# Optimization experiments

Measured on AMD Instinct MI355X. Metric: run time of the kernel, lower is better.

The kernel has to match this reference:

```python
import jax, jax.numpy as jnp
import numpy as np
import math

B, S, D, H, F = 2, 2048, 1024, 16, 4096
HD = D // H  # head size 64
EPS = 1e-5


def layernorm(x, g, b):
    mu = jnp.mean(x, axis=-1, keepdims=True)
    var = jnp.mean((x - mu) ** 2, axis=-1, keepdims=True)
    return (x - mu) * jax.lax.rsqrt(var + EPS) * g + b


def new_gelu(x):
    c = math.sqrt(2.0 / math.pi)
    return 0.5 * x * (1.0 + jnp.tanh(c * (x + 0.044715 * x ** 3)))


def setup_inputs() -> dict:
    key = jax.random.key(0)
    ks = jax.random.split(key, 20)
    sc = 0.02
    return {
        "x": jax.random.normal(ks[0], (B, S, D), jnp.float32),
        # per-head q/k/v weights stacked: [H, HD, D] (torch Linear weight layout [out,in])
        "Wq": jax.random.normal(ks[1], (H, HD, D), jnp.float32) * sc,
        "bq": jax.random.normal(ks[2], (H, HD), jnp.float32) * sc,
        "Wk": jax.random.normal(ks[3], (H, HD, D), jnp.float32) * sc,
        "bk": jax.random.normal(ks[4], (H, HD), jnp.float32) * sc,
        "Wv": jax.random.normal(ks[5], (H, HD, D), jnp.float32) * sc,
        "bv": jax.random.normal(ks[6], (H, HD), jnp.float32) * sc,
        "Wo": jax.random.normal(ks[7], (D, D), jnp.float32) * sc,
        "bo": jax.random.normal(ks[8], (D,), jnp.float32) * sc,
        "ln1_g": 1.0 + jax.random.normal(ks[9], (D,), jnp.float32) * sc,
        "ln1_b": jax.random.normal(ks[10], (D,), jnp.float32) * sc,
        "W1": jax.random.normal(ks[11], (F, D), jnp.float32) * sc,
        "b1": jax.random.normal(ks[12], (F,), jnp.float32) * sc,
        "W2": jax.random.normal(ks[13], (D, F), jnp.float32) * sc,
        "b2": jax.random.normal(ks[14], (D,), jnp.float32) * sc,
        "ln2_g": 1.0 + jax.random.normal(ks[15], (D,), jnp.float32) * sc,
        "ln2_b": jax.random.normal(ks[16], (D,), jnp.float32) * sc,
    }


def reference(x, Wq, bq, Wk, bk, Wv, bv, Wo, bo, ln1_g, ln1_b, W1, b1, W2, b2, ln2_g, ln2_b):
    # --- pre-LN multi-head attention (dropout is identity in eval) ---
    h = layernorm(x, ln1_g, ln1_b)
    q = jnp.einsum("bsd,hed->bshe", h, Wq) + bq  # [B,S,H,HD]
    k = jnp.einsum("bsd,hed->bshe", h, Wk) + bk
    v = jnp.einsum("bsd,hed->bshe", h, Wv) + bv
    scores = jnp.einsum("bshe,bthe->bhst", q, k) / math.sqrt(HD)
    probs = jax.nn.softmax(scores, axis=-1)
    attn = jnp.einsum("bhst,bthe->bshe", probs, v).reshape(B, S, D)  # concat heads
    attn = attn @ Wo.T + bo
    x = x + attn
    # --- pre-LN MLP with NewGELU ---
    h2 = layernorm(x, ln2_g, ln2_b)
    mlp = new_gelu(h2 @ W1.T + b1) @ W2.T + b2
    return x + mlp
```

## Files before the change

kernel.cpp:

```cpp
#include <hip/hip_runtime.h>

typedef unsigned short u16;
typedef __attribute__((ext_vector_type(8))) __bf16 bf16x8;
typedef __attribute__((ext_vector_type(4))) __bf16 bf16x4;
typedef __attribute__((ext_vector_type(4))) float f32x4;
typedef __attribute__((ext_vector_type(4))) unsigned short u16x4;

#define AS1 __attribute__((address_space(1)))
#define AS3 __attribute__((address_space(3)))

__device__ __forceinline__ void async_load16(const void* g, void* l) {
  __builtin_amdgcn_global_load_lds((const AS1 void*)g, (AS3 void*)l, 16, 0, 0);
}

__device__ __forceinline__ float exp2_fast(float x) {
#if __has_builtin(__builtin_amdgcn_exp2f)
  return __builtin_amdgcn_exp2f(x);
#else
  return exp2f(x);
#endif
}
__device__ __forceinline__ float rcp_fast(float x) {
#if __has_builtin(__builtin_amdgcn_rcpf)
  return __builtin_amdgcn_rcpf(x);
#else
  return 1.0f / x;
#endif
}

__device__ __forceinline__ u16 f2bf(float f) {
  union { float f; unsigned u; } a; a.f = f;
  unsigned u = a.u;
  u += 0x7fffu + ((u >> 16) & 1u);
  return (u16)(u >> 16);
}
__device__ __forceinline__ u16 bf_bits(float f) {
  union { __bf16 b; u16 u; } c; c.b = (__bf16)f; return c.u;
}
__device__ __forceinline__ float bf2f(u16 h) {
  union { unsigned u; float f; } c; c.u = ((unsigned)h) << 16; return c.f;
}

__global__ __launch_bounds__(256)
void f2b_all(const float* __restrict__ s0, const float* __restrict__ s1,
             const float* __restrict__ s2, const float* __restrict__ s3,
             const float* __restrict__ s4, const float* __restrict__ s5,
             u16* __restrict__ dst) {
  const int i = blockIdx.x * 256 + threadIdx.x;
  const float* s; int off;
  if (i < 1048576) {
    if (i < 262144)      { s = s0; off = i; }
    else if (i < 524288) { s = s1; off = i - 262144; }
    else if (i < 786432) { s = s2; off = i - 524288; }
    else                 { s = s3; off = i - 786432; }
  } else if (i < 2097152) { s = s4; off = i - 1048576; }
  else                    { s = s5; off = i - 2097152; }
  const float4 v = ((const float4*)s)[off];
  u16x4 o; o[0] = f2bf(v.x); o[1] = f2bf(v.y); o[2] = f2bf(v.z); o[3] = f2bf(v.w);
  ((u16x4*)dst)[i] = o;
}

__global__ __launch_bounds__(256)
void ln_kernel(const float* __restrict__ x, const float* __restrict__ g,
               const float* __restrict__ b, u16* __restrict__ out) {
  const int row = blockIdx.x, tid = threadIdx.x;
  const float4 v = ((const float4*)(x + (size_t)row * 1024))[tid];
  float s = v.x + v.y + v.z + v.w;
  float s2 = v.x * v.x + v.y * v.y + v.z * v.z + v.w * v.w;
#pragma unroll
  for (int o = 1; o < 64; o <<= 1) { s += __shfl_xor(s, o); s2 += __shfl_xor(s2, o); }
  __shared__ float red[8];
  const int wave = tid >> 6, lane = tid & 63;
  if (lane == 0) { red[wave] = s; red[wave + 4] = s2; }
  __syncthreads();
  s = red[0] + red[1] + red[2] + red[3];
  s2 = red[4] + red[5] + red[6] + red[7];
  const float mu = s * (1.f / 1024.f);
  const float rstd = rsqrtf(s2 * (1.f / 1024.f) - mu * mu + 1e-5f);
  const float4 gg = ((const float4*)g)[tid];
  const float4 bb = ((const float4*)b)[tid];
  u16x4 o4;
  o4[0] = f2bf((v.x - mu) * rstd * gg.x + bb.x);
  o4[1] = f2bf((v.y - mu) * rstd * gg.y + bb.y);
  o4[2] = f2bf((v.z - mu) * rstd * gg.z + bb.z);
  o4[3] = f2bf((v.w - mu) * rstd * gg.w + bb.w);
  ((u16x4*)(out + (size_t)row * 1024))[tid] = o4;
}

__global__ __launch_bounds__(256)
void ln_fuse(const float* __restrict__ x, const u16* __restrict__ parts,
             const float* __restrict__ bo, const float* __restrict__ g,
             const float* __restrict__ b, float* __restrict__ out,
             u16* __restrict__ hb) {
  const int row = blockIdx.x, tid = threadIdx.x;
  const size_t base = (size_t)row * 1024;
  const int i4 = row * 256 + tid;
  const float4 xv = ((const float4*)(x + base))[tid];
  const u16x4 h0 = ((const u16x4*)parts)[i4];
  const u16x4 h1 = ((const u16x4*)(parts + 4194304))[i4];
  const float4 bv = ((const float4*)bo)[tid];
  float4 t;
  t.x = xv.x + bf2f(h0[0]) + bf2f(h1[0]) + bv.x;
  t.y = xv.y + bf2f(h0[1]) + bf2f(h1[1]) + bv.y;
  t.z = xv.z + bf2f(h0[2]) + bf2f(h1[2]) + bv.z;
  t.w = xv.w + bf2f(h0[3]) + bf2f(h1[3]) + bv.w;
  ((float4*)(out + base))[tid] = t;
  float s = t.x + t.y + t.z + t.w;
  float s2 = t.x * t.x + t.y * t.y + t.z * t.z + t.w * t.w;
#pragma unroll
  for (int o = 1; o < 64; o <<= 1) { s += __shfl_xor(s, o); s2 += __shfl_xor(s2, o); }
  __shared__ float red[8];
  const int wave = tid >> 6, lane = tid & 63;
  if (lane == 0) { red[wave] = s; red[wave + 4] = s2; }
  __syncthreads();
  s = red[0] + red[1] + red[2] + red[3];
  s2 = red[4] + red[5] + red[6] + red[7];
  const float mu = s * (1.f / 1024.f);
  const float rstd = rsqrtf(s2 * (1.f / 1024.f) - mu * mu + 1e-5f);
  const float4 gg = ((const float4*)g)[tid];
  const float4 bb = ((const float4*)b)[tid];
  u16x4 o4;
  o4[0] = f2bf((t.x - mu) * rstd * gg.x + bb.x);
  o4[1] = f2bf((t.y - mu) * rstd * gg.y + bb.y);
  o4[2] = f2bf((t.z - mu) * rstd * gg.z + bb.z);
  o4[3] = f2bf((t.w - mu) * rstd * gg.w + bb.w);
  ((u16x4*)(hb + base))[tid] = o4;
}

__global__ __launch_bounds__(256)
void add4(float* __restrict__ out, const u16* __restrict__ p,
          const float* __restrict__ b2) {
  const int i = blockIdx.x * 256 + threadIdx.x;
  const float4 o = ((const float4*)out)[i];
  const float4 bv = ((const float4*)b2)[i & 255];
  float a0 = o.x + bv.x, a1 = o.y + bv.y, a2 = o.z + bv.z, a3 = o.w + bv.w;
#pragma unroll
  for (int kz = 0; kz < 4; kz++) {
    const u16x4 h = ((const u16x4*)(p + (size_t)kz * 4194304))[i];
    a0 += bf2f(h[0]); a1 += bf2f(h[1]); a2 += bf2f(h[2]); a3 += bf2f(h[3]);
  }
  float4 r; r.x = a0; r.y = a1; r.z = a2; r.w = a3;
  ((float4*)out)[i] = r;
}

template <class Epi>
__global__ __launch_bounds__(256)
void gemm_bt(const u16* __restrict__ A, const u16* __restrict__ Bw,
             int ldk, int K, Epi epi) {
  __shared__ __align__(16) u16 As[128 * 32];
  __shared__ __align__(16) u16 Bs[128 * 32];
  const int tid = threadIdx.x;
  const int wave = tid >> 6, lane = tid & 63;
  const int quad = lane >> 4, l16 = lane & 15;
  const int bm = blockIdx.x * 128, bn = blockIdx.y * 128;
  const int kz = blockIdx.z;
  const int wm = (wave & 1) * 64, wn = (wave >> 1) * 64;

  const int srow = lane >> 2, scol = (lane & 3) * 8;
  const u16* pa0 = A + (size_t)(bm + wave * 32 + srow) * ldk + (size_t)kz * K + scol;
  const u16* pa1 = pa0 + (size_t)16 * ldk;
  const u16* pb0 = Bw + (size_t)(bn + wave * 32 + srow) * ldk + (size_t)kz * K + scol;
  const u16* pb1 = pb0 + (size_t)16 * ldk;
  u16* la0 = &As[wave * 1024];
  u16* la1 = la0 + 512;
  u16* lb0 = &Bs[wave * 1024];
  u16* lb1 = lb0 + 512;

  const f32x4 fz = {0.f, 0.f, 0.f, 0.f};
  f32x4 acc[4][4];
#pragma unroll
  for (int i = 0; i < 4; i++)
#pragma unroll
    for (int j = 0; j < 4; j++) acc[i][j] = fz;

  for (int k0 = 0; k0 < K; k0 += 32) {
    async_load16(pa0, la0);
    async_load16(pa1, la1);
    async_load16(pb0, lb0);
    async_load16(pb1, lb1);
    pa0 += 32; pa1 += 32; pb0 += 32; pb1 += 32;
    __syncthreads();
    bf16x8 af[4], bfr[4];
#pragma unroll
    for (int mi = 0; mi < 4; mi++)
      af[mi] = *(const bf16x8*)&As[(wm + mi * 16 + l16) * 32 + quad * 8];
#pragma unroll
    for (int ni = 0; ni < 4; ni++)
      bfr[ni] = *(const bf16x8*)&Bs[(wn + ni * 16 + l16) * 32 + quad * 8];
#pragma unroll
    for (int mi = 0; mi < 4; mi++)
#pragma unroll
      for (int ni = 0; ni < 4; ni++)
        acc[mi][ni] = __builtin_amdgcn_mfma_f32_16x16x32_bf16(af[mi], bfr[ni], acc[mi][ni], 0, 0, 0);
    __syncthreads();
  }
#pragma unroll
  for (int mi = 0; mi < 4; mi++)
#pragma unroll
    for (int ni = 0; ni < 4; ni++)
      epi(bm + wm + mi * 16 + quad * 4, bn + wn + ni * 16 + l16, kz, acc[mi][ni]);
}

struct EpiQKV {
  u16 *q, *k, *vt; const float *bq, *bk, *bv;
  __device__ void operator()(int m0, int n, int, f32x4 v) const {
    const int which = n >> 10, nn = n & 1023;
    const int hh = nn >> 6, e = nn & 63;
    const int bb = m0 >> 11, s0 = m0 & 2047;
    const size_t bh = (size_t)(bb * 16 + hh);
    if (which == 0) {
      const float bias = bq[nn];
      u16* p = &q[(bh * 2048 + s0) * 64 + e];
#pragma unroll
      for (int r = 0; r < 4; r++) p[r * 64] = bf_bits((v[r] + bias) * 0.18033688f);
    } else if (which == 1) {
      const float bias = bk[nn];
      u16* p = &k[(bh * 2048 + s0) * 64 + e];
#pragma unroll
      for (int r = 0; r < 4; r++) p[r * 64] = bf_bits(v[r] + bias);
    } else {
      const float bias = bv[nn];
      bf16x4 pk;
#pragma unroll
      for (int r = 0; r < 4; r++) pk[r] = (__bf16)(v[r] + bias);
      *(bf16x4*)&vt[(bh * 64 + e) * 2048 + s0] = pk;
    }
  }
};
struct EpiPartB {
  u16* p;
  __device__ void operator()(int m0, int n, int kz, f32x4 v) const {
    u16* pp = p + (size_t)kz * 4194304;
#pragma unroll
    for (int r = 0; r < 4; r++) pp[(size_t)(m0 + r) * 1024 + n] = bf_bits(v[r]);
  }
};
struct EpiGelu {
  const float* b1; u16* o;
  __device__ void operator()(int m0, int n, int, f32x4 v) const {
    const float bias = b1[n];
#pragma unroll
    for (int r = 0; r < 4; r++) {
      const float u = v[r] + bias;
      const float z2 = u * (2.3021183f + 0.10294515f * u * u);
      const float d = 1.0f + exp2_fast(-z2);
      o[(size_t)(m0 + r) * 4096 + n] = bf_bits(u * rcp_fast(d));
    }
  }
};

__global__ __launch_bounds__(256)
void attn_kernel(const u16* __restrict__ Q, const u16* __restrict__ K,
                 const u16* __restrict__ Vt, u16* __restrict__ O) {
  __shared__ __align__(16) u16 Ks[64 * 72];
  __shared__ __align__(16) u16 Vs[64 * 72];
  __shared__ __align__(16) u16 Ps[4][32 * 72];
  const int tid = threadIdx.x, wave = tid >> 6, lane = tid & 63;
  const int quad = lane >> 4, l16 = lane & 15;
  const int b = blockIdx.z, h = blockIdx.y, qt = blockIdx.x;
  const size_t bh = (size_t)(b * 16 + h);
  const u16* Qp = Q + bh * (size_t)(2048 * 64);
  const u16* Kp = K + bh * (size_t)(2048 * 64);
  const u16* Vp = Vt + bh * (size_t)(64 * 2048);
  const int q0 = qt * 128 + wave * 32;

  bf16x8 qf[2][2];
#pragma unroll
  for (int rg = 0; rg < 2; rg++) {
    const u16* qrow = &Qp[(size_t)(q0 + rg * 16 + l16) * 64 + quad * 8];
    qf[rg][0] = *(const bf16x8*)qrow;
    qf[rg][1] = *(const bf16x8*)(qrow + 32);
  }

  const int sr = tid >> 2, sc = (tid & 3) * 16;
  const int krow = 4 * (sr & 15) + (sr >> 4);
  const u16* kg = &Kp[(size_t)krow * 64 + sc];
  const u16* vg = &Vp[(size_t)sr * 2048 + sc];
  u16* kl = &Ks[sr * 72 + sc];
  u16* vl = &Vs[sr * 72 + sc];
  u16* Pw = &Ps[wave][0];

  bf16x8 ones;
#pragma unroll
  for (int i = 0; i < 8; i++) ones[i] = (__bf16)1.0f;

  const f32x4 fz = {0.f, 0.f, 0.f, 0.f};
  f32x4 acc[2][4], lsum[2];
#pragma unroll
  for (int rg = 0; rg < 2; rg++) {
    lsum[rg] = fz;
#pragma unroll
    for (int g = 0; g < 4; g++) acc[rg][g] = fz;
  }

  bf16x8 pk0 = *(const bf16x8*)kg, pk1 = *(const bf16x8*)(kg + 8);
  bf16x8 pv0 = *(const bf16x8*)vg, pv1 = *(const bf16x8*)(vg + 8);

  for (int t0 = 0; t0 < 2048; t0 += 64) {
    *(bf16x8*)kl = pk0; *(bf16x8*)(kl + 8) = pk1;
    *(bf16x8*)vl = pv0; *(bf16x8*)(vl + 8) = pv1;
    __syncthreads();
    kg += 64 * 64; vg += 64;
    pk0 = *(const bf16x8*)kg; pk1 = *(const bf16x8*)(kg + 8);
    pv0 = *(const bf16x8*)vg; pv1 = *(const bf16x8*)(vg + 8);

    f32x4 s[2][4];
#pragma unroll
    for (int g = 0; g < 4; g++) {
      const u16* kr = &Ks[(g * 16 + l16) * 72 + quad * 8];
      const bf16x8 kb0 = *(const bf16x8*)kr;
      const bf16x8 kb1 = *(const bf16x8*)(kr + 32);
#pragma unroll
      for (int rg = 0; rg < 2; rg++) {
        f32x4 z = __builtin_amdgcn_mfma_f32_16x16x32_bf16(qf[rg][0], kb0, fz, 0, 0, 0);
        s[rg][g] = __builtin_amdgcn_mfma_f32_16x16x32_bf16(qf[rg][1], kb1, z, 0, 0, 0);
      }
    }
#pragma unroll
    for (int rg = 0; rg < 2; rg++)
#pragma unroll
      for (int r = 0; r < 4; r++) {
        f32x4 pf;
#pragma unroll
        for (int g = 0; g < 4; g++) pf[g] = exp2_fast(s[rg][g][r]);
        const bf16x4 pb = __builtin_convertvector(pf, bf16x4);
        *(bf16x4*)&Pw[(rg * 16 + quad * 4 + r) * 72 + 4 * l16] = pb;
      }
    bf16x8 pa[2][2];
#pragma unroll
    for (int rg = 0; rg < 2; rg++) {
      const u16* pr = &Pw[(rg * 16 + l16) * 72 + quad * 8];
      pa[rg][0] = *(const bf16x8*)pr;
      pa[rg][1] = *(const bf16x8*)(pr + 32);
      lsum[rg] = __builtin_amdgcn_mfma_f32_16x16x32_bf16(pa[rg][0], ones, lsum[rg], 0, 0, 0);
      lsum[rg] = __builtin_amdgcn_mfma_f32_16x16x32_bf16(pa[rg][1], ones, lsum[rg], 0, 0, 0);
    }
#pragma unroll
    for (int g = 0; g < 4; g++) {
      const u16* vr = &Vs[(g * 16 + l16) * 72 + quad * 8];
      const bf16x8 vb0 = *(const bf16x8*)vr;
      const bf16x8 vb1 = *(const bf16x8*)(vr + 32);
#pragma unroll
      for (int rg = 0; rg < 2; rg++) {
        acc[rg][g] = __builtin_amdgcn_mfma_f32_16x16x32_bf16(pa[rg][0], vb0, acc[rg][g], 0, 0, 0);
        acc[rg][g] = __builtin_amdgcn_mfma_f32_16x16x32_bf16(pa[rg][1], vb1, acc[rg][g], 0, 0, 0);
      }
    }
    __syncthreads();
  }
#pragma unroll
  for (int rg = 0; rg < 2; rg++)
#pragma unroll
    for (int r = 0; r < 4; r++) {
      const float inv = rcp_fast(lsum[rg][r]);
      const int s_row = q0 + rg * 16 + quad * 4 + r;
      u16* op = (u16*)&O[((size_t)(b * 2048 + s_row)) * 1024 + h * 64 + l16];
#pragma unroll
      for (int g = 0; g < 4; g++) op[g * 16] = bf_bits(acc[rg][g][r] * inv);
    }
}

extern "C" void kernel_launch(void* const* d_in, const int* in_sizes, int n_in,
                              void* d_out, int out_size, void* d_ws, size_t ws_size,
                              hipStream_t stream) {
  const float* x   = (const float*)d_in[0];
  const float* Wq  = (const float*)d_in[1];
  const float* bq  = (const float*)d_in[2];
  const float* Wk  = (const float*)d_in[3];
  const float* bk  = (const float*)d_in[4];
  const float* Wv  = (const float*)d_in[5];
  const float* bv  = (const float*)d_in[6];
  const float* Wo  = (const float*)d_in[7];
  const float* bo  = (const float*)d_in[8];
  const float* g1  = (const float*)d_in[9];
  const float* be1 = (const float*)d_in[10];
  const float* W1  = (const float*)d_in[11];
  const float* b1  = (const float*)d_in[12];
  const float* W2  = (const float*)d_in[13];
  const float* b2  = (const float*)d_in[14];
  const float* g2  = (const float*)d_in[15];
  const float* be2 = (const float*)d_in[16];
  float* out = (float*)d_out;

  char* w = (char*)d_ws;
  u16* wqkv = (u16*)w; w += (size_t)3072 * 1024 * 2;
  u16* wob  = (u16*)w; w += (size_t)1024 * 1024 * 2;
  u16* w1b  = (u16*)w; w += (size_t)4096 * 1024 * 2;
  u16* w2b  = (u16*)w; w += (size_t)1024 * 4096 * 2;
  u16* hb   = (u16*)w; w += (size_t)4096 * 1024 * 2;
  u16* qb   = (u16*)w; w += (size_t)4096 * 1024 * 2;
  u16* kb   = (u16*)w; w += (size_t)4096 * 1024 * 2;
  u16* vtb  = (u16*)w; w += (size_t)4096 * 1024 * 2;
  u16* atb  = (u16*)w; w += (size_t)4096 * 1024 * 2;
  u16* m1b  = (u16*)w; w += (size_t)4096 * 4096 * 2;

  u16* op_part = m1b;
  u16* ml_part = qb;

  f2b_all<<<12288, 256, 0, stream>>>(Wq, Wk, Wv, Wo, W1, W2, wqkv);

  ln_kernel<<<4096, 256, 0, stream>>>(x, g1, be1, hb);
  gemm_bt<EpiQKV><<<dim3(32, 24, 1), 256, 0, stream>>>(hb, wqkv, 1024, 1024,
      EpiQKV{qb, kb, vtb, bq, bk, bv});
  attn_kernel<<<dim3(16, 16, 2), 256, 0, stream>>>(qb, kb, vtb, atb);
  gemm_bt<EpiPartB><<<dim3(32, 8, 2), 256, 0, stream>>>(atb, wob, 1024, 512,
      EpiPartB{op_part});
  ln_fuse<<<4096, 256, 0, stream>>>(x, op_part, bo, g2, be2, out, hb);
  gemm_bt<EpiGelu><<<dim3(32, 32, 1), 256, 0, stream>>>(hb, w1b, 1024, 1024,
      EpiGelu{b1, m1b});
  gemm_bt<EpiPartB><<<dim3(32, 8, 4), 256, 0, stream>>>(m1b, w2b, 4096, 1024,
      EpiPartB{ml_part});
  add4<<<4096, 256, 0, stream>>>(out, ml_part, b2);
}
```

Measured before the change: 385.6 us.

## Enlarge GEMM tile to 256x128 with M-fastest 1D block swizzle

The GEMM block tile grows from 128x128 to 256x128, with each wave computing a 64x128 sub-tile (4x8 MFMA accumulators). This raises arithmetic intensity per LDS load and per global fetch. The grid becomes 1D with M-blocks varying fastest, so consecutive blocks share the same B (weight) tile for L2 reuse. Costs are more accumulator registers, a launch_bounds occupancy hint of 2, and fewer blocks (256-512) to fill the CUs.

```diff
diff --git a/kernel.cpp b/kernel.cpp
--- a/kernel.cpp
+++ b/kernel.cpp
@@ -144,61 +144,70 @@
 }
 
 template <class Epi>
-__global__ __launch_bounds__(256)
+__global__ __launch_bounds__(256, 2)
 void gemm_bt(const u16* __restrict__ A, const u16* __restrict__ Bw,
-             int ldk, int K, Epi epi) {
-  __shared__ __align__(16) u16 As[128 * 32];
+             int ldk, int K, int NB, Epi epi) {
+  __shared__ __align__(16) u16 As[256 * 32];
   __shared__ __align__(16) u16 Bs[128 * 32];
   const int tid = threadIdx.x;
   const int wave = tid >> 6, lane = tid & 63;
   const int quad = lane >> 4, l16 = lane & 15;
-  const int bm = blockIdx.x * 128, bn = blockIdx.y * 128;
-  const int kz = blockIdx.z;
-  const int wm = (wave & 1) * 64, wn = (wave >> 1) * 64;
+  const int id = blockIdx.x;
+  const int mb = id & 15;
+  const int t = id >> 4;
+  const int nb = t % NB;
+  const int kz = t / NB;
+  const int bm = mb * 256, bn = nb * 128;
+  const int wm = wave * 64;
 
   const int srow = lane >> 2, scol = (lane & 3) * 8;
-  const u16* pa0 = A + (size_t)(bm + wave * 32 + srow) * ldk + (size_t)kz * K + scol;
-  const u16* pa1 = pa0 + (size_t)16 * ldk;
-  const u16* pb0 = Bw + (size_t)(bn + wave * 32 + srow) * ldk + (size_t)kz * K + scol;
-  const u16* pb1 = pb0 + (size_t)16 * ldk;
-  u16* la0 = &As[wave * 1024];
-  u16* la1 = la0 + 512;
-  u16* lb0 = &Bs[wave * 1024];
-  u16* lb1 = lb0 + 512;
+  const u16* pa[4];
+  u16* la[4];
+#pragma unroll
+  for (int j = 0; j < 4; j++) {
+    pa[j] = A + (size_t)(bm + wave * 64 + j * 16 + srow) * ldk + (size_t)kz * K + scol;
+    la[j] = &As[wave * 2048 + j * 512];
+  }
+  const u16* pb[2];
+  u16* lb[2];
+#pragma unroll
+  for (int j = 0; j < 2; j++) {
+    pb[j] = Bw + (size_t)(bn + wave * 32 + j * 16 + srow) * ldk + (size_t)kz * K + scol;
+    lb[j] = &Bs[wave * 1024 + j * 512];
+  }
 
   const f32x4 fz = {0.f, 0.f, 0.f, 0.f};
-  f32x4 acc[4][4];
+  f32x4 acc[4][8];
 #pragma unroll
   for (int i = 0; i < 4; i++)
 #pragma unroll
-    for (int j = 0; j < 4; j++) acc[i][j] = fz;
+    for (int j = 0; j < 8; j++) acc[i][j] = fz;
 
   for (int k0 = 0; k0 < K; k0 += 32) {
-    async_load16(pa0, la0);
-    async_load16(pa1, la1);
-    async_load16(pb0, lb0);
-    async_load16(pb1, lb1);
-    pa0 += 32; pa1 += 32; pb0 += 32; pb1 += 32;
+#pragma unroll
+    for (int j = 0; j < 4; j++) { async_load16(pa[j], la[j]); pa[j] += 32; }
+#pragma unroll
+    for (int j = 0; j < 2; j++) { async_load16(pb[j], lb[j]); pb[j] += 32; }
     __syncthreads();
-    bf16x8 af[4], bfr[4];
+    bf16x8 af[4], bfr[8];
 #pragma unroll
     for (int mi = 0; mi < 4; mi++)
       af[mi] = *(const bf16x8*)&As[(wm + mi * 16 + l16) * 32 + quad * 8];
 #pragma unroll
-    for (int ni = 0; ni < 4; ni++)
-      bfr[ni] = *(const bf16x8*)&Bs[(wn + ni * 16 + l16) * 32 + quad * 8];
+    for (int ni = 0; ni < 8; ni++)
+      bfr[ni] = *(const bf16x8*)&Bs[(ni * 16 + l16) * 32 + quad * 8];
 #pragma unroll
     for (int mi = 0; mi < 4; mi++)
 #pragma unroll
-      for (int ni = 0; ni < 4; ni++)
+      for (int ni = 0; ni < 8; ni++)
         acc[mi][ni] = __builtin_amdgcn_mfma_f32_16x16x32_bf16(af[mi], bfr[ni], acc[mi][ni], 0, 0, 0);
     __syncthreads();
   }
 #pragma unroll
   for (int mi = 0; mi < 4; mi++)
 #pragma unroll
-    for (int ni = 0; ni < 4; ni++)
-      epi(bm + wm + mi * 16 + quad * 4, bn + wn + ni * 16 + l16, kz, acc[mi][ni]);
+    for (int ni = 0; ni < 8; ni++)
+      epi(bm + wm + mi * 16 + quad * 4, bn + ni * 16 + l16, kz, acc[mi][ni]);
 }
 
 struct EpiQKV {
@@ -400,15 +409,15 @@
   f2b_all<<<12288, 256, 0, stream>>>(Wq, Wk, Wv, Wo, W1, W2, wqkv);
 
   ln_kernel<<<4096, 256, 0, stream>>>(x, g1, be1, hb);
-  gemm_bt<EpiQKV><<<dim3(32, 24, 1), 256, 0, stream>>>(hb, wqkv, 1024, 1024,
+  gemm_bt<EpiQKV><<<384, 256, 0, stream>>>(hb, wqkv, 1024, 1024, 24,
       EpiQKV{qb, kb, vtb, bq, bk, bv});
   attn_kernel<<<dim3(16, 16, 2), 256, 0, stream>>>(qb, kb, vtb, atb);
-  gemm_bt<EpiPartB><<<dim3(32, 8, 2), 256, 0, stream>>>(atb, wob, 1024, 512,
+  gemm_bt<EpiPartB><<<256, 256, 0, stream>>>(atb, wob, 1024, 512, 8,
       EpiPartB{op_part});
   ln_fuse<<<4096, 256, 0, stream>>>(x, op_part, bo, g2, be2, out, hb);
-  gemm_bt<EpiGelu><<<dim3(32, 32, 1), 256, 0, stream>>>(hb, w1b, 1024, 1024,
+  gemm_bt<EpiGelu><<<512, 256, 0, stream>>>(hb, w1b, 1024, 1024, 32,
       EpiGelu{b1, m1b});
-  gemm_bt<EpiPartB><<<dim3(32, 8, 4), 256, 0, stream>>>(m1b, w2b, 4096, 1024,
+  gemm_bt<EpiPartB><<<512, 256, 0, stream>>>(m1b, w2b, 4096, 1024, 8,
       EpiPartB{ml_part});
   add4<<<4096, 256, 0, stream>>>(out, ml_part, b2);
 }
```

After: 359.4 us. 6.8% less time.
